# Optimization experiments

Hardware: AMD Instinct MI355X
Metric: run time of the kernel (lower is better)

The kernel has to match this reference:

```python
import jax, jax.numpy as jnp
import numpy as np

DICT_LEN = 9
NUM_LS = 8
DIM = 1024
SEQ = 2048
BZ = 32


def setup_inputs() -> dict:
    key = jax.random.key(0)
    k_x, k_ids, k_w, k_b = jax.random.split(key, 4)
    x = jax.random.normal(k_x, (SEQ, BZ, DIM), dtype=jnp.float32)
    lang_ids = jax.random.randint(k_ids, (BZ,), 0, DICT_LEN)
    # torch nn.Linear init: U(-1/sqrt(in), 1/sqrt(in)), weight shape [out, in]
    bound = 1.0 / np.sqrt(DIM)
    W = jax.random.uniform(k_w, (NUM_LS, DIM, DIM), dtype=jnp.float32, minval=-bound, maxval=bound)
    b = jax.random.uniform(k_b, (NUM_LS, DIM), dtype=jnp.float32, minval=-bound, maxval=bound)
    return {"x": x, "lang_ids": lang_ids, "W": W, "b": b}


def reference(x, lang_ids, W, b):
    # Mapper.forward: gid = dict_len - 1 - lang_ids; tokens with gid in [1, num_ls]
    # are transformed by Linear #(gid-1); all other batch columns pass through.
    gid = DICT_LEN - 1 - lang_ids                      # [bz]
    active = (gid >= 1) & (gid <= NUM_LS)              # [bz]
    eidx = jnp.clip(gid - 1, 0, NUM_LS - 1)            # [bz] expert index (dummy 0 where inactive)
    We = W[eidx]                                       # [bz, dim, dim] (torch Linear weight layout [out, in])
    be = b[eidx]                                       # [bz, dim]
    y = jnp.einsum("sbd,bed->sbe", x, We) + be[None, :, :]
    return jnp.where(active[None, :, None], y, x)
```

## Files before the change

### kernel.cpp

```cpp
#include <hip/hip_runtime.h>
#include <hip/hip_bf16.h>

#define TSEQ 2048
#define TBZ  32
#define TDIM 1024
#define NLS  8

typedef __attribute__((ext_vector_type(8))) short bf16x8;
typedef __attribute__((ext_vector_type(4))) float f32x4;

__device__ inline unsigned int pk2(float lo, float hi) {
    __hip_bfloat162 h = __float22bfloat162_rn(make_float2(lo, hi));
    return *reinterpret_cast<const unsigned int*>(&h);
}

__device__ inline void gload_lds16(const void* g, void* l) {
    __builtin_amdgcn_global_load_lds(
        (const __attribute__((address_space(1))) unsigned int*)g,
        (__attribute__((address_space(3))) unsigned int*)l,
        16, 0, 0);
}

__global__ __launch_bounds__(256) void conv_pre(
    const float* __restrict__ x, const int* __restrict__ lang_ids,
    const float* __restrict__ W,
    unsigned short* __restrict__ xb, unsigned short* __restrict__ wb,
    int* __restrict__ flags)
{
    const int bid = blockIdx.x;
    if (bid == 512) {
        if (threadIdx.x < 256) flags[threadIdx.x] = 0;
        return;
    }
    if (bid < 256) {
        const int total = NLS * TDIM * TDIM / 8;
        for (int i = bid * 256 + threadIdx.x; i < total; i += 256 * 256) {
            const float* src = W + (long)i * 8;
            f32x4 v0 = *(const f32x4*)(src);
            f32x4 v1 = *(const f32x4*)(src + 4);
            uint4 o;
            o.x = pk2(v0.x, v0.y); o.y = pk2(v0.z, v0.w);
            o.z = pk2(v1.x, v1.y); o.w = pk2(v1.z, v1.w);
            *(uint4*)(wb + (long)i * 8) = o;
        }
        return;
    }
    const int i  = bid - 256;
    const int c  = i >> 2;
    const int q  = i & 3;
    const int b  = c >> 1;
    const int gid = 8 - lang_ids[b];
    if (!(gid >= 1 && gid <= 8)) return;
    const int srow0 = (c & 1) * 4 * 256 + q * 64;
    for (int r = 0; r < 64; ++r) {
        const int s = srow0 + r;
        const float* sp = x + ((long)s * TBZ + b) * TDIM + threadIdx.x * 4;
        f32x4 v = *(const f32x4*)sp;
        uint2 o; o.x = pk2(v.x, v.y); o.y = pk2(v.z, v.w);
        *(uint2*)(xb + ((long)b * TSEQ + s) * TDIM + threadIdx.x * 4) = o;
    }
}


#define BAR __builtin_amdgcn_s_barrier()
#define SB0 __builtin_amdgcn_sched_barrier(0)
#define VMC(n) asm volatile("s_waitcnt vmcnt(" #n ")" ::: "memory")
#define KAo(kv) (((kv) & 1023) + (((kv) >> 10) << 18))
#define KBo(kv) ((kv) & 1023)

__global__ __launch_bounds__(512, 2) void mapper_gemm8p(
    const float* __restrict__ x,
    unsigned short* xb,
    const int* __restrict__ lang_ids,
    const unsigned short* __restrict__ wb,
    const float* __restrict__ bias,
    int* flags,
    float* __restrict__ out)
{
    const int p  = blockIdx.x;
    const int l  = (p & 7) * 32 + (p >> 3);
    const int b  = l >> 3;
    const int strip = (l >> 2) & 1;
    const int nt = l & 3;
    const int s0 = strip * 1024;
    const int e0 = nt * 256;
    const int tid = threadIdx.x;

    const int gid = 8 - lang_ids[b];
    if (!(gid >= 1 && gid <= 8)) {
        const f32x4* xs = (const f32x4*)x;
        f32x4*       os = (f32x4*)out;
        const int rs4 = TBZ * TDIM / 4;
        for (int i = tid; i < 1024 * 256 / 4; i += 512) {
            int r = i >> 6;
            int c = i & 63;
            long idx = (long)(s0 + r) * rs4 + b * (TDIM / 4) + (e0 >> 2) + c;
            os[idx] = xs[idx];
        }
        return;
    }
    const int eb = gid - 1;

    __shared__ uint4 ldsbuf[131072 / 16];
    char* ldsc = (char*)ldsbuf;

    const int lane = tid & 63;
    const int wave = tid >> 6;
    const int wr   = wave >> 2;
    const int wc   = wave & 3;
    const int fr   = lane & 15;
    const int fq   = lane >> 4;
    const int fr7  = fr & 7;

    const unsigned short* Aab = xb + (long)b  * TSEQ * TDIM + (long)s0 * TDIM;
    const unsigned short* __restrict__ Bbb = wb + (long)eb * TDIM * TDIM + (long)e0 * TDIM;

    const int L    = lane;
    const int lch8 = ((L & 7) ^ (L >> 3)) * 8;
    const int ldA0 = wave * 2048 + L * 16;
    const unsigned short* aG[2][2];
    const unsigned short* bG[2][2];
    #pragma unroll
    for (int j = 0; j < 2; ++j) {
        const int rr = wave * 16 + j * 8 + (L >> 3);
        #pragma unroll
        for (int mh = 0; mh < 2; ++mh)
            aG[j][mh] = Aab + ((rr >> 6) * 128 + mh * 64 + (rr & 63)) * TDIM + lch8;
        #pragma unroll
        for (int nh = 0; nh < 2; ++nh)
            bG[j][nh] = Bbb + ((rr >> 5) * 64 + nh * 32 + (rr & 31)) * TDIM + lch8;
    }

#define STAGE_A(slot, mh, kofs) do { \
    gload_lds16(aG[0][mh] + (kofs), ldsc + (slot)*32768 + (mh)*16384 + ldA0); \
    gload_lds16(aG[1][mh] + (kofs), ldsc + (slot)*32768 + (mh)*16384 + ldA0 + 1024); \
} while (0)
#define STAGE_B(slot, nh, kofs) do { \
    gload_lds16(bG[0][nh] + (kofs), ldsc + 65536 + (slot)*32768 + (nh)*16384 + ldA0); \
    gload_lds16(bG[1][nh] + (kofs), ldsc + 65536 + (slot)*32768 + (nh)*16384 + ldA0 + 1024); \
} while (0)
#define RD_A(slot, mh) do { \
    _Pragma("unroll") for (int ml = 0; ml < 4; ++ml) { \
        const int rr = wr * 64 + ml * 16 + fr; \
        _Pragma("unroll") for (int kk = 0; kk < 2; ++kk) \
            af[ml][kk] = *(const bf16x8*)(ldsc + (slot)*32768 + (mh)*16384 + rr*128 + (((kk*4+fq) ^ fr7) << 4)); \
    } } while (0)
#define RD_B(slot, nh, br) do { \
    _Pragma("unroll") for (int nl = 0; nl < 2; ++nl) { \
        const int rr = wc * 32 + nl * 16 + fr; \
        _Pragma("unroll") for (int kk = 0; kk < 2; ++kk) \
            br[nl][kk] = *(const bf16x8*)(ldsc + 65536 + (slot)*32768 + (nh)*16384 + rr*128 + (((kk*4+fq) ^ fr7) << 4)); \
    } } while (0)
#define MM(mh, nh, br) do { \
    __builtin_amdgcn_s_setprio(1); \
    _Pragma("unroll") for (int ml = 0; ml < 4; ++ml) \
    _Pragma("unroll") for (int nl = 0; nl < 2; ++nl) \
    _Pragma("unroll") for (int kk = 0; kk < 2; ++kk) \
        acc[(mh)*4+ml][(nh)*2+nl] = __builtin_amdgcn_mfma_f32_16x16x32_bf16( \
            br[nl][kk], af[ml][kk], acc[(mh)*4+ml][(nh)*2+nl], 0, 0, 0); \
    __builtin_amdgcn_s_setprio(0); \
} while (0)

#define CONVQ(mt) do { \
    const int sbase_ = (mt) * 256 + nt * 64 + wave * 8; \
    _Pragma("unroll 1") for (int r_ = 0; r_ < 8; ++r_) { \
        const int s_ = sbase_ + r_; \
        const float* sp_ = x + ((long)s_ * TBZ + b) * TDIM + lane * 16; \
        f32x4 a0_ = *(const f32x4*)(sp_);      f32x4 a1_ = *(const f32x4*)(sp_ + 4); \
        f32x4 a2_ = *(const f32x4*)(sp_ + 8);  f32x4 a3_ = *(const f32x4*)(sp_ + 12); \
        uint4 o0_, o1_; \
        o0_.x = pk2(a0_.x, a0_.y); o0_.y = pk2(a0_.z, a0_.w); \
        o0_.z = pk2(a1_.x, a1_.y); o0_.w = pk2(a1_.z, a1_.w); \
        o1_.x = pk2(a2_.x, a2_.y); o1_.y = pk2(a2_.z, a2_.w); \
        o1_.z = pk2(a3_.x, a3_.y); o1_.w = pk2(a3_.z, a3_.w); \
        unsigned short* dp_ = xb + ((long)b * TSEQ + s_) * TDIM + lane * 16; \
        *(uint4*)(dp_)     = o0_; \
        *(uint4*)(dp_ + 8) = o1_; \
    } \
} while (0)

    f32x4 acc[8][4];
    #pragma unroll
    for (int m = 0; m < 8; ++m)
        #pragma unroll
        for (int n = 0; n < 4; ++n)
            acc[m][n] = (f32x4){0.f, 0.f, 0.f, 0.f};

    bf16x8 af[4][2], bf0[2][2], bf1[2][2];

    const int flbase = (b * 2 + strip) * 4;

    STAGE_A(0, 0, 0);  STAGE_B(0, 0, 0);  STAGE_B(0, 1, 0);  STAGE_A(0, 1, 0);
    STAGE_A(1, 0, 64); STAGE_B(1, 0, 64); STAGE_B(1, 1, 64);
    VMC(6); BAR; SB0;

    const int cs  = lane & 15;
    const int eqb = (lane >> 4) << 2;

    #pragma unroll 1
    for (int mtl = 0; mtl < 4; ++mtl) {
        #pragma unroll 1
        for (int it = 0; it < 8; ++it) {
            if (it == 7 && mtl < 3) {
                if (lane == 0) {
                    while (__hip_atomic_load(&flags[flbase + mtl + 1],
                                             __ATOMIC_RELAXED,
                                             __HIP_MEMORY_SCOPE_AGENT) < 4)
                        __builtin_amdgcn_s_sleep(2);
                }
                __hip_atomic_load(&flags[flbase + mtl + 1],
                                  __ATOMIC_ACQUIRE, __HIP_MEMORY_SCOPE_AGENT);
                SB0;
            }
            const int kva = mtl * 1024 + it * 128;
            const int kb = kva + 64;
            const int kn = kva + 128;
            const int km = kva + 192;
            RD_A(0, 0); RD_B(0, 0, bf0); STAGE_A(1, 1, KAo(kb));
            BAR; SB0; MM(0, 0, bf0); BAR; SB0;
            RD_B(0, 1, bf1); STAGE_A(0, 0, KAo(kn));
            BAR; SB0; MM(0, 1, bf1); BAR; SB0;
            RD_A(0, 1); STAGE_B(0, 0, KBo(kn));
            BAR; SB0; MM(1, 0, bf0); BAR; SB0;
            STAGE_B(0, 1, KBo(kn));
            BAR; SB0; MM(1, 1, bf1); VMC(6);
            if (it == 1 && mtl < 3 && tid == 0)
                __hip_atomic_fetch_add(&flags[flbase + mtl + 1], 1,
                                       __ATOMIC_RELEASE, __HIP_MEMORY_SCOPE_AGENT);
            BAR; SB0;
            RD_A(1, 0); RD_B(1, 0, bf0); STAGE_A(0, 1, KAo(kn));
            BAR; SB0; MM(0, 0, bf0); BAR; SB0;
            RD_B(1, 1, bf1); STAGE_A(1, 0, KAo(km));
            BAR; SB0; MM(0, 1, bf1); BAR; SB0;
            RD_A(1, 1); STAGE_B(1, 0, KBo(km));
            BAR; SB0; MM(1, 0, bf0); BAR; SB0;
            STAGE_B(1, 1, KBo(km));
            BAR; SB0; MM(1, 1, bf1); VMC(6); SB0;
            if (it == 0 && mtl < 3) { CONVQ(strip * 4 + mtl + 1); }
            BAR; SB0;
        }

        const int sb = s0 + mtl * 256 + wr * 128;
        #pragma unroll
        for (int n = 0; n < 4; ++n) {
            const int e = e0 + wc * 64 + n * 16 + eqb;
            const f32x4 bv4 = *(const f32x4*)&bias[eb * TDIM + e];
            #pragma unroll
            for (int m = 0; m < 8; ++m) {
                const int s = sb + m * 16 + cs;
                *(f32x4*)&out[(long)s * (TBZ * TDIM) + b * TDIM + e] = acc[m][n] + bv4;
            }
        }
        #pragma unroll
        for (int m = 0; m < 8; ++m)
            #pragma unroll
            for (int n = 0; n < 4; ++n)
                acc[m][n] = (f32x4){0.f, 0.f, 0.f, 0.f};
    }
#undef STAGE_A
#undef STAGE_B
#undef RD_A
#undef RD_B
#undef MM
#undef CONVQ
}

__device__ inline unsigned short f2bf(float f) {
    union { float f; unsigned int u; } v; v.f = f;
    unsigned int r = v.u + 0x7fffu + ((v.u >> 16) & 1u);
    return (unsigned short)(r >> 16);
}
constexpr int FLDS = 40;

__global__ __launch_bounds__(256) void mapper_fused(
    const float* __restrict__ x, const int* __restrict__ lang_ids,
    const float* __restrict__ W, const float* __restrict__ bias,
    float* __restrict__ out)
{
    const int bid = blockIdx.x;
    const int b   = bid >> 7;
    const int t   = bid & 127;
    const int mt  = t >> 3;
    const int nt  = t & 7;
    const int s0  = mt * 128;
    const int e0  = nt * 128;
    const int tid = threadIdx.x;

    const int gid = 8 - lang_ids[b];
    const bool active = (gid >= 1) && (gid <= 8);
    int eb = gid - 1; eb = eb < 0 ? 0 : (eb > 7 ? 7 : eb);

    if (!active) {
        const f32x4* xs = (const f32x4*)x;
        f32x4*       os = (f32x4*)out;
        const int rs4 = TBZ * TDIM / 4;
        for (int i = tid; i < 128 * 128 / 4; i += 256) {
            int r = i >> 5, c = i & 31;
            long idx = (long)(s0 + r) * rs4 + b * (TDIM / 4) + (e0 >> 2) + c;
            os[idx] = xs[idx];
        }
        return;
    }

    __shared__ unsigned short As[128 * FLDS];
    __shared__ unsigned short Bs[128 * FLDS];
    const float* __restrict__ Wb = W + (long)eb * TDIM * TDIM;

    const int lane = tid & 63;
    const int wave = tid >> 6;
    const int wrr  = wave >> 1;
    const int wcc  = wave & 1;

    f32x4 acc[4][4];
    #pragma unroll
    for (int m = 0; m < 4; ++m)
        #pragma unroll
        for (int n = 0; n < 4; ++n)
            acc[m][n] = (f32x4){0.f, 0.f, 0.f, 0.f};

    const int rg = tid >> 3;
    const int cg = tid & 7;
    const int fr = lane & 15;
    const int fo = (lane >> 4) * 8;

    for (int k0 = 0; k0 < TDIM; k0 += 32) {
        __syncthreads();
        #pragma unroll
        for (int pp = 0; pp < 4; ++pp) {
            const int r = rg + pp * 32;
            f32x4 av = *(const f32x4*)(x  + (long)(s0 + r) * (TBZ * TDIM) + b * TDIM + k0 + cg * 4);
            f32x4 bv = *(const f32x4*)(Wb + (long)(e0 + r) * TDIM + k0 + cg * 4);
            unsigned int alo = (unsigned)f2bf(av.x) | ((unsigned)f2bf(av.y) << 16);
            unsigned int ahi = (unsigned)f2bf(av.z) | ((unsigned)f2bf(av.w) << 16);
            unsigned int blo = (unsigned)f2bf(bv.x) | ((unsigned)f2bf(bv.y) << 16);
            unsigned int bhi = (unsigned)f2bf(bv.z) | ((unsigned)f2bf(bv.w) << 16);
            *(uint2*)&As[r * FLDS + cg * 4] = make_uint2(alo, ahi);
            *(uint2*)&Bs[r * FLDS + cg * 4] = make_uint2(blo, bhi);
        }
        __syncthreads();

        bf16x8 af2[4], bfm[4];
        #pragma unroll
        for (int m = 0; m < 4; ++m)
            af2[m] = *(const bf16x8*)&As[(wrr * 64 + m * 16 + fr) * FLDS + fo];
        #pragma unroll
        for (int n = 0; n < 4; ++n)
            bfm[n] = *(const bf16x8*)&Bs[(wcc * 64 + n * 16 + fr) * FLDS + fo];
        #pragma unroll
        for (int m = 0; m < 4; ++m)
            #pragma unroll
            for (int n = 0; n < 4; ++n)
                acc[m][n] = __builtin_amdgcn_mfma_f32_16x16x32_bf16(af2[m], bfm[n], acc[m][n], 0, 0, 0);
    }

    const int cr = lane >> 4;
    const int cc2 = lane & 15;
    #pragma unroll
    for (int n = 0; n < 4; ++n) {
        const int e  = e0 + wcc * 64 + n * 16 + cc2;
        const float bv = bias[eb * TDIM + e];
        #pragma unroll
        for (int m = 0; m < 4; ++m) {
            #pragma unroll
            for (int j = 0; j < 4; ++j) {
                const int s = s0 + wrr * 64 + m * 16 + cr * 4 + j;
                out[(long)s * (TBZ * TDIM) + b * TDIM + e] = acc[m][n][j] + bv;
            }
        }
    }
}

extern "C" void kernel_launch(void* const* d_in, const int* in_sizes, int n_in,
                              void* d_out, int out_size, void* d_ws, size_t ws_size,
                              hipStream_t stream) {
    const float* x        = (const float*)d_in[0];
    const int*   lang_ids = (const int*)d_in[1];
    const float* W        = (const float*)d_in[2];
    const float* bias     = (const float*)d_in[3];
    float*       out      = (float*)d_out;

    const size_t xbytes = (size_t)TSEQ * TBZ * TDIM * 2;
    const size_t wbytes = (size_t)NLS * TDIM * TDIM * 2;
    const size_t fbytes = 1024;

    if (ws_size >= xbytes + wbytes + fbytes) {
        unsigned short* xbp = (unsigned short*)d_ws;
        unsigned short* wbp = (unsigned short*)((char*)d_ws + xbytes);
        int*            flg = (int*)((char*)d_ws + xbytes + wbytes);
        conv_pre<<<513, 256, 0, stream>>>(x, lang_ids, W, xbp, wbp, flg);
        mapper_gemm8p<<<256, 512, 0, stream>>>(x, xbp, lang_ids, wbp, bias, flg, out);
    } else {
        mapper_fused<<<TBZ * 16 * 8, 256, 0, stream>>>(x, lang_ids, W, bias, out);
    }
}
```

Baseline: 302.6 us.

## Offload x bf16 conversion to dedicated producer waves in GEMM kernel

Adds two extra waves per block (640 threads) that convert upcoming fp32 x rows to bf16 and signal readiness through the flags. The conversion work is removed from the MFMA compute waves. The producer waves match the compute waves' barrier count so block barriers stay aligned. This aims to overlap conversion with matrix math instead of stalling compute waves. The cost is a larger block, a dropped min-blocks launch bound that may change register allocation and occupancy, and fragile barrier matching.

```diff
diff --git a/kernel.cpp b/kernel.cpp
--- a/kernel.cpp
+++ b/kernel.cpp
@@ -68,7 +68,7 @@
 #define KAo(kv) (((kv) & 1023) + (((kv) >> 10) << 18))
 #define KBo(kv) ((kv) & 1023)
 
-__global__ __launch_bounds__(512, 2) void mapper_gemm8p(
+__global__ __launch_bounds__(640) void mapper_gemm8p(
     const float* __restrict__ x,
     unsigned short* xb,
     const int* __restrict__ lang_ids,
@@ -91,7 +91,7 @@
         const f32x4* xs = (const f32x4*)x;
         f32x4*       os = (f32x4*)out;
         const int rs4 = TBZ * TDIM / 4;
-        for (int i = tid; i < 1024 * 256 / 4; i += 512) {
+        for (int i = tid; i < 1024 * 256 / 4; i += 640) {
             int r = i >> 6;
             int c = i & 63;
             long idx = (long)(s0 + r) * rs4 + b * (TDIM / 4) + (e0 >> 2) + c;
@@ -106,6 +106,46 @@
 
     const int lane = tid & 63;
     const int wave = tid >> 6;
+    const int flbase = (b * 2 + strip) * 4;
+
+    if (wave >= 8) {
+        const int cw = wave - 8;
+        BAR;
+        #pragma unroll 1
+        for (int mtl = 0; mtl < 4; ++mtl) {
+            #pragma unroll 1
+            for (int it = 0; it < 8; ++it) {
+                #pragma unroll 1
+                for (int k = 0; k < 16; ++k) {
+                    if (mtl < 3 && it < 2) {
+                        const int mt = strip * 4 + mtl + 1;
+                        const int r0 = mt * 256 + nt * 64 + it * 32 + k * 2;
+                        #pragma unroll
+                        for (int j = 0; j < 2; ++j) {
+                            const int s = r0 + j;
+                            const float* sp = x + ((long)s * TBZ + b) * TDIM
+                                                + cw * 512 + lane * 8;
+                            f32x4 v0 = *(const f32x4*)sp;
+                            f32x4 v1 = *(const f32x4*)(sp + 4);
+                            uint4 o;
+                            o.x = pk2(v0.x, v0.y); o.y = pk2(v0.z, v0.w);
+                            o.z = pk2(v1.x, v1.y); o.w = pk2(v1.z, v1.w);
+                            *(uint4*)(xb + ((long)b * TSEQ + s) * TDIM
+                                         + cw * 512 + lane * 8) = o;
+                        }
+                    }
+                    if (mtl < 3 && it == 2 && k == 0) { VMC(0); }
+                    BAR;
+                    if (mtl < 3 && it == 2 && k == 0 && cw == 0 && lane == 0)
+                        __hip_atomic_fetch_add(&flags[flbase + mtl + 1], 1,
+                                               __ATOMIC_RELEASE,
+                                               __HIP_MEMORY_SCOPE_AGENT);
+                }
+            }
+        }
+        return;
+    }
+
     const int wr   = wave >> 2;
     const int wc   = wave & 3;
     const int fr   = lane & 15;
@@ -161,24 +201,6 @@
     __builtin_amdgcn_s_setprio(0); \
 } while (0)
 
-#define CONVQ(mt) do { \
-    const int sbase_ = (mt) * 256 + nt * 64 + wave * 8; \
-    _Pragma("unroll 1") for (int r_ = 0; r_ < 8; ++r_) { \
-        const int s_ = sbase_ + r_; \
-        const float* sp_ = x + ((long)s_ * TBZ + b) * TDIM + lane * 16; \
-        f32x4 a0_ = *(const f32x4*)(sp_);      f32x4 a1_ = *(const f32x4*)(sp_ + 4); \
-        f32x4 a2_ = *(const f32x4*)(sp_ + 8);  f32x4 a3_ = *(const f32x4*)(sp_ + 12); \
-        uint4 o0_, o1_; \
-        o0_.x = pk2(a0_.x, a0_.y); o0_.y = pk2(a0_.z, a0_.w); \
-        o0_.z = pk2(a1_.x, a1_.y); o0_.w = pk2(a1_.z, a1_.w); \
-        o1_.x = pk2(a2_.x, a2_.y); o1_.y = pk2(a2_.z, a2_.w); \
-        o1_.z = pk2(a3_.x, a3_.y); o1_.w = pk2(a3_.z, a3_.w); \
-        unsigned short* dp_ = xb + ((long)b * TSEQ + s_) * TDIM + lane * 16; \
-        *(uint4*)(dp_)     = o0_; \
-        *(uint4*)(dp_ + 8) = o1_; \
-    } \
-} while (0)
-
     f32x4 acc[8][4];
     #pragma unroll
     for (int m = 0; m < 8; ++m)
@@ -187,8 +209,6 @@
             acc[m][n] = (f32x4){0.f, 0.f, 0.f, 0.f};
 
     bf16x8 af[4][2], bf0[2][2], bf1[2][2];
-
-    const int flbase = (b * 2 + strip) * 4;
 
     STAGE_A(0, 0, 0);  STAGE_B(0, 0, 0);  STAGE_B(0, 1, 0);  STAGE_A(0, 1, 0);
     STAGE_A(1, 0, 64); STAGE_B(1, 0, 64); STAGE_B(1, 1, 64);
@@ -223,11 +243,7 @@
             RD_A(0, 1); STAGE_B(0, 0, KBo(kn));
             BAR; SB0; MM(1, 0, bf0); BAR; SB0;
             STAGE_B(0, 1, KBo(kn));
-            BAR; SB0; MM(1, 1, bf1); VMC(6);
-            if (it == 1 && mtl < 3 && tid == 0)
-                __hip_atomic_fetch_add(&flags[flbase + mtl + 1], 1,
-                                       __ATOMIC_RELEASE, __HIP_MEMORY_SCOPE_AGENT);
-            BAR; SB0;
+            BAR; SB0; MM(1, 1, bf1); VMC(6); BAR; SB0;
             RD_A(1, 0); RD_B(1, 0, bf0); STAGE_A(0, 1, KAo(kn));
             BAR; SB0; MM(0, 0, bf0); BAR; SB0;
             RD_B(1, 1, bf1); STAGE_A(1, 0, KAo(km));
@@ -235,9 +251,7 @@
             RD_A(1, 1); STAGE_B(1, 0, KBo(km));
             BAR; SB0; MM(1, 0, bf0); BAR; SB0;
             STAGE_B(1, 1, KBo(km));
-            BAR; SB0; MM(1, 1, bf1); VMC(6); SB0;
-            if (it == 0 && mtl < 3) { CONVQ(strip * 4 + mtl + 1); }
-            BAR; SB0;
+            BAR; SB0; MM(1, 1, bf1); VMC(6); BAR; SB0;
         }
 
         const int sb = s0 + mtl * 256 + wr * 128;
@@ -262,7 +276,6 @@
 #undef RD_A
 #undef RD_B
 #undef MM
-#undef CONVQ
 }
 
 __device__ inline unsigned short f2bf(float f) {
@@ -388,7 +401,7 @@
         unsigned short* wbp = (unsigned short*)((char*)d_ws + xbytes);
         int*            flg = (int*)((char*)d_ws + xbytes + wbytes);
         conv_pre<<<513, 256, 0, stream>>>(x, lang_ids, W, xbp, wbp, flg);
-        mapper_gemm8p<<<256, 512, 0, stream>>>(x, xbp, lang_ids, wbp, bias, flg, out);
+        mapper_gemm8p<<<256, 640, 0, stream>>>(x, xbp, lang_ids, wbp, bias, flg, out);
     } else {
         mapper_fused<<<TBZ * 16 * 8, 256, 0, stream>>>(x, lang_ids, W, bias, out);
     }
```

Result: slower. 947.7 us (+213.2%).
